# Performance work log

Measured on AMD Instinct MI355X. Metric: run time of the kernel, lower is better.

## Reference

```python
import jax, jax.numpy as jnp
import numpy as np

B, S, H = 2, 1024, 1024
E, I, K = 16, 512, 4
SHARED_I = 512 * 2  # moe_intermediate_size * moe_num_shared_experts
NORM_MIN = 1e-12


def _mlp(x, gw, uw, dw):
    # gated SiLU MLP: down(silu(gate(x)) * up(x))
    return (jax.nn.silu(x @ gw) * (x @ uw)) @ dw


def setup_inputs() -> dict:
    key = jax.random.key(0)
    ks = jax.random.split(key, 9)
    s = 0.02
    return {
        "hidden_states": jax.random.normal(ks[0], (B, S, H), jnp.float32),
        "gate_weight": jax.random.normal(ks[1], (H, E), jnp.float32) * s,
        "corr_bias": jnp.zeros((E,), jnp.float32),
        "gate_w": jax.random.normal(ks[2], (E, H, I), jnp.float32) * s,
        "up_w": jax.random.normal(ks[3], (E, H, I), jnp.float32) * s,
        "down_w": jax.random.normal(ks[4], (E, I, H), jnp.float32) * s,
        "shared_gate_w": jax.random.normal(ks[5], (H, SHARED_I), jnp.float32) * s,
        "shared_up_w": jax.random.normal(ks[6], (H, SHARED_I), jnp.float32) * s,
        "shared_down_w": jax.random.normal(ks[7], (SHARED_I, H), jnp.float32) * s,
    }


def reference(hidden_states, gate_weight, corr_bias, gate_w, up_w, down_w,
              shared_gate_w, shared_up_w, shared_down_w):
    b, s, h = hidden_states.shape
    x = hidden_states.reshape(-1, h)                      # [T, H]
    T = x.shape[0]

    # shared experts (full-capacity, always applied)
    shared_out = _mlp(x, shared_gate_w, shared_up_w, shared_down_w)

    # router in float32
    router_logits = x.astype(jnp.float32) @ gate_weight   # [T, E]
    probs = jax.nn.softmax(router_logits, axis=-1)
    # top-k on bias-corrected scores, weights gathered from uncorrected probs
    _, selected = jax.lax.top_k(probs + corr_bias[None, :], K)  # [T, K]
    rw = jnp.take_along_axis(probs, selected, axis=-1)          # [T, K]
    rw = rw / jnp.maximum(rw.sum(-1, keepdims=True), NORM_MIN)
    rw = rw.astype(x.dtype)

    # dense combine weights [T, E] (zero for unselected experts)
    cw = jnp.zeros((T, gate_weight.shape[1]), x.dtype)
    cw = cw.at[jnp.arange(T)[:, None], selected].add(rw)

    # grouped expert MLPs (full capacity, no token dropping)
    g = jnp.einsum('th,ehi->tei', x, gate_w)
    u = jnp.einsum('th,ehi->tei', x, up_w)
    eo = jnp.einsum('tei,eih->teh', jax.nn.silu(g) * u, down_w)
    final = jnp.einsum('teh,te->th', eo, cw) + shared_out

    return final.reshape(b, s, h), router_logits
```

## Files before the change

kernel.cpp:

```cpp
#include <hip/hip_runtime.h>
#include <hip/hip_bf16.h>

#define T_TOK 2048
#define H_DIM 1024
#define E_NUM 16
#define I_DIM 512
#define K_TOP 4
#define SI_DIM 1024

typedef __bf16 bf16x8 __attribute__((ext_vector_type(8)));
typedef __bf16 bf16x4 __attribute__((ext_vector_type(4)));
typedef float f32x4 __attribute__((ext_vector_type(4)));

#define GL2L(g, l)                                                                       \
  __builtin_amdgcn_global_load_lds((const __attribute__((address_space(1))) void*)(g),   \
                                   (__attribute__((address_space(3))) void*)(l), 16, 0, 0)
#define BAR() __builtin_amdgcn_s_barrier()

__global__ __launch_bounds__(256) void transpose_all_kernel(
    const float* __restrict__ gate_w, const float* __restrict__ up_w,
    const float* __restrict__ down_w, const float* __restrict__ sgw,
    const float* __restrict__ suw, const float* __restrict__ sdw,
    const float* __restrict__ gate_weight, __bf16* __restrict__ gw_t,
    __bf16* __restrict__ uw_t, __bf16* __restrict__ dw_t, __bf16* __restrict__ sgw_t,
    __bf16* __restrict__ suw_t, __bf16* __restrict__ sdw_t, float* __restrict__ gwt_f) {
  int tid = threadIdx.x;
  if (blockIdx.x >= 1728) {
    int b = blockIdx.x - 1728;
#pragma unroll
    for (int k = 0; k < 4; k++) {
      int idx = k * 4096 + b * 256 + tid;
      gwt_f[idx] = gate_weight[(idx & 1023) * E_NUM + (idx >> 10)];
    }
    return;
  }
  __shared__ float tile[64][65];
  for (int t = blockIdx.x; t < 6912; t += 1728) {
    const float* in;
    __bf16* out;
    int R, C, r0, c0;
    if (t < 4096) {
      bool g = t < 2048;
      int b = t & 2047;
      int z = b >> 7;
      int ti = b & 127;
      R = H_DIM;
      C = I_DIM;
      r0 = (ti >> 3) * 64;
      c0 = (ti & 7) * 64;
      size_t off = (size_t)z * R * C;
      in = (g ? gate_w : up_w) + off;
      out = (g ? gw_t : uw_t) + off;
    } else if (t < 6144) {
      int b = t - 4096;
      int z = b >> 7;
      int ti = b & 127;
      R = I_DIM;
      C = H_DIM;
      r0 = (ti >> 4) * 64;
      c0 = (ti & 15) * 64;
      size_t off = (size_t)z * R * C;
      in = down_w + off;
      out = dw_t + off;
    } else {
      int b = t - 6144;
      int m = b >> 8;
      int ti = b & 255;
      R = 1024;
      C = 1024;
      r0 = (ti >> 4) * 64;
      c0 = (ti & 15) * 64;
      in = m == 0 ? sgw : m == 1 ? suw : sdw;
      out = m == 0 ? sgw_t : m == 1 ? suw_t : sdw_t;
    }
#pragma unroll
    for (int q = 0; q < 4; q++) {
      int lin = q * 256 + tid;
      int row = lin >> 4, c4 = (lin & 15) * 4;
      float4 v = *(const float4*)(in + (size_t)(r0 + row) * C + c0 + c4);
      tile[row][c4] = v.x;
      tile[row][c4 + 1] = v.y;
      tile[row][c4 + 2] = v.z;
      tile[row][c4 + 3] = v.w;
    }
    __syncthreads();
    int c = tid >> 2, rb = (tid & 3) * 16;
    bf16x8 lo, hi;
#pragma unroll
    for (int i = 0; i < 8; i++) lo[i] = (__bf16)tile[rb + i][c];
#pragma unroll
    for (int i = 0; i < 8; i++) hi[i] = (__bf16)tile[rb + 8 + i][c];
    __bf16* op = out + (size_t)(c0 + c) * R + r0 + rb;
    *(bf16x8*)op = lo;
    *(bf16x8*)(op + 8) = hi;
    __syncthreads();
  }
}

__global__ __launch_bounds__(256) void router_kernel(
    const float* __restrict__ x, const float* __restrict__ gwt, const float* __restrict__ cbias,
    float* __restrict__ logits_out, __bf16* __restrict__ x_bf, int* __restrict__ selE,
    float* __restrict__ selW) {
  int t = blockIdx.x;
  int tid = threadIdx.x;
  int wid = tid >> 6, lane = tid & 63;
  int e = lane >> 2, cl = lane & 3;
  int c = wid * 4 + cl;
  const float* xr = x + (size_t)t * H_DIM + c * 64;
  const float* gr = gwt + (size_t)e * H_DIM + c * 64;
  float a0 = 0.f, a1 = 0.f, a2 = 0.f, a3 = 0.f;
#pragma unroll
  for (int j = 0; j < 16; j++) {
    float4 xv = *(const float4*)(xr + j * 4);
    float4 gv = *(const float4*)(gr + j * 4);
    if (e == 0) {
      bf16x4 o = {(__bf16)xv.x, (__bf16)xv.y, (__bf16)xv.z, (__bf16)xv.w};
      *(bf16x4*)(x_bf + (size_t)t * H_DIM + c * 64 + j * 4) = o;
    }
    a0 = fmaf(xv.x, gv.x, a0);
    a1 = fmaf(xv.y, gv.y, a1);
    a2 = fmaf(xv.z, gv.z, a2);
    a3 = fmaf(xv.w, gv.w, a3);
  }
  float a = (a0 + a1) + (a2 + a3);
  a += __shfl_xor(a, 1);
  a += __shfl_xor(a, 2);
  __shared__ float part[4][16];
  if (cl == 0) part[wid][e] = a;
  __syncthreads();
  if (wid != 0) return;
  float logit = -1e30f;
  if (lane < E_NUM)
    logit = (part[0][lane] + part[1][lane]) + (part[2][lane] + part[3][lane]);
  if (lane < E_NUM) logits_out[(size_t)t * E_NUM + lane] = logit;
  float m = logit;
#pragma unroll
  for (int mk = 8; mk >= 1; mk >>= 1) m = fmaxf(m, __shfl_xor(m, mk));
  float p = __expf(logit - m);
  float s = p;
#pragma unroll
  for (int mk = 8; mk >= 1; mk >>= 1) s += __shfl_xor(s, mk);
  p /= s;
  float score = (lane < E_NUM) ? p + cbias[lane] : -1e30f;
  int sel[K_TOP];
  float w[K_TOP];
#pragma unroll
  for (int k = 0; k < K_TOP; k++) {
    float bv = score;
    int bi = (lane < E_NUM) ? lane : 999;
#pragma unroll
    for (int mk = 1; mk <= 8; mk <<= 1) {
      float ov = __shfl_xor(bv, mk);
      int oi = __shfl_xor(bi, mk);
      if (ov > bv || (ov == bv && oi < bi)) {
        bv = ov;
        bi = oi;
      }
    }
    sel[k] = bi;
    w[k] = __shfl(p, bi);
    if (lane == bi) score = -1e30f;
  }
  if (lane == 0) {
    float wsum = fmaxf(w[0] + w[1] + w[2] + w[3], 1e-12f);
#pragma unroll
    for (int k = 0; k < K_TOP; k++) {
      selE[t * K_TOP + k] = sel[k];
      selW[t * K_TOP + k] = w[k] / wsum;
    }
  }
}

__global__ __launch_bounds__(1024) void count_place_kernel(
    const int* __restrict__ selE, int* __restrict__ counts, int* __restrict__ offs,
    int* __restrict__ slot_of_tk, int* __restrict__ tok_of_slot) {
  int tid = threadIdx.x;
  int wv = tid >> 6, lane = tid & 63;
  unsigned long long lt = (1ULL << lane) - 1ULL;
  __shared__ int wcnt[16][16];
  __shared__ int wbase[16][16];
  __shared__ int glob[16];
  __shared__ int offsh[16];
  if (tid < 16) glob[tid] = 0;
  __syncthreads();
  int ex[8], rk[8];
#pragma unroll
  for (int r = 0; r < 8; r++) {
    int e = selE[r * 1024 + tid];
    ex[r] = e;
    int rank = 0;
#pragma unroll
    for (int q = 0; q < 16; q++) {
      unsigned long long b = __ballot(e == q);
      int c = __popcll(b & lt);
      if (e == q) rank = c;
      if (lane == q) wcnt[wv][q] = __popcll(b);
    }
    __syncthreads();
    if (wv == 0 && lane < 16) {
      int run = glob[lane];
#pragma unroll
      for (int w = 0; w < 16; w++) {
        wbase[w][lane] = run;
        run += wcnt[w][lane];
      }
      glob[lane] = run;
    }
    __syncthreads();
    rk[r] = rank + wbase[wv][e];
    __syncthreads();
  }
  if (wv == 0 && lane == 0) {
    int s = 0;
#pragma unroll
    for (int q = 0; q < 16; q++) {
      offsh[q] = s;
      s += glob[q];
    }
  }
  __syncthreads();
  if (tid < 16) {
    counts[tid] = glob[tid];
    offs[tid] = offsh[tid];
  }
#pragma unroll
  for (int r = 0; r < 8; r++) {
    int entry = r * 1024 + tid;
    int slot = offsh[ex[r]] + rk[r];
    slot_of_tk[entry] = slot;
    tok_of_slot[slot] = entry >> 2;
  }
}

__global__ __launch_bounds__(256, 3) void gemm_stage1(
    const __bf16* __restrict__ x_bf, const int* __restrict__ tok_of_slot,
    const int* __restrict__ counts, const int* __restrict__ offs, const __bf16* __restrict__ gw_t,
    const __bf16* __restrict__ uw_t, const __bf16* __restrict__ sgw_t,
    const __bf16* __restrict__ suw_t, __bf16* __restrict__ he, __bf16* __restrict__ hs) {
  __shared__ __align__(16) __bf16 Alds[128 * 64];
  __shared__ __align__(16) __bf16 Bgl[2 * 64 * 64];
  __shared__ __align__(16) __bf16 Bul[2 * 64 * 64];
  int z = blockIdx.z, bx = blockIdx.x, m0 = blockIdx.y * 128;
  const __bf16 *Bg, *Bu;
  __bf16* Cp;
  const int* tokIdx;
  int rowOff, M, ldC, n0;
  if (z < E_NUM) {
    M = counts[z];
    if (m0 >= M) return;
    tokIdx = tok_of_slot;
    rowOff = offs[z];
    Bg = gw_t + (size_t)z * I_DIM * H_DIM;
    Bu = uw_t + (size_t)z * I_DIM * H_DIM;
    Cp = he;
    ldC = I_DIM;
    n0 = bx * 64;
  } else {
    tokIdx = nullptr;
    rowOff = 0;
    M = T_TOK;
    Bg = sgw_t;
    Bu = suw_t;
    Cp = hs;
    ldC = SI_DIM;
    n0 = (z - E_NUM) * 512 + bx * 64;
  }
  int tid = threadIdx.x;
  int wave = tid >> 6, lane = tid & 63;
  int rsub = lane >> 3, chunk = lane & 7;
  int sch = (chunk ^ rsub) * 8;
  size_t aB[4], bB[2];
#pragma unroll
  for (int j = 0; j < 4; j++) {
    int r = wave * 32 + j * 8 + rsub;
    int ar = m0 + r;
    ar = ar < M - 1 ? ar : M - 1;
    int grow = tokIdx ? tokIdx[rowOff + ar] : rowOff + ar;
    aB[j] = (size_t)grow * H_DIM + sch;
  }
#pragma unroll
  for (int j = 0; j < 2; j++) {
    int r = wave * 16 + j * 8 + rsub;
    bB[j] = (size_t)(n0 + r) * H_DIM + sch;
  }
  int wm = (wave >> 1) * 64, wn = (wave & 1) * 32;
  int rl = lane & 15, gq = lane >> 4;
  int xa = rl & 7;

  auto STAGE_A = [&](int k0) {
#pragma unroll
    for (int j = 0; j < 4; j++) GL2L(x_bf + aB[j] + k0, Alds + (wave * 32 + j * 8) * 64);
  };
  auto STAGE_B = [&](int k0, int buf) {
#pragma unroll
    for (int j = 0; j < 2; j++) {
      int ld = buf * 4096 + (wave * 16 + j * 8) * 64;
      GL2L(Bg + bB[j] + k0, Bgl + ld);
      GL2L(Bu + bB[j] + k0, Bul + ld);
    }
  };

  f32x4 accg[4][2] = {}, accu[4][2] = {};
  const int NT = H_DIM / 64;
  STAGE_A(0);
  STAGE_B(0, 0);
  int buf = 0;
  for (int t = 0; t < NT; ++t) {
    if (t + 1 < NT) {
      STAGE_B((t + 1) << 6, buf ^ 1);
      asm volatile("s_waitcnt vmcnt(4)" ::: "memory");
    } else {
      asm volatile("s_waitcnt vmcnt(0)" ::: "memory");
    }
    BAR();
    const __bf16* Bgr = Bgl + buf * 4096;
    const __bf16* Bur = Bul + buf * 4096;
#pragma unroll
    for (int s = 0; s < 2; s++) {
      int lc = ((s * 4 + gq) ^ xa) * 8;
      bf16x8 af[4], bg[2], bu[2];
#pragma unroll
      for (int m = 0; m < 4; m++) af[m] = *(const bf16x8*)&Alds[(wm + m * 16 + rl) * 64 + lc];
#pragma unroll
      for (int n = 0; n < 2; n++) {
        bg[n] = *(const bf16x8*)&Bgr[(wn + n * 16 + rl) * 64 + lc];
        bu[n] = *(const bf16x8*)&Bur[(wn + n * 16 + rl) * 64 + lc];
      }
#pragma unroll
      for (int m = 0; m < 4; m++)
#pragma unroll
        for (int n = 0; n < 2; n++) {
          accg[m][n] =
              __builtin_amdgcn_mfma_f32_16x16x32_bf16(af[m], bg[n], accg[m][n], 0, 0, 0);
          accu[m][n] =
              __builtin_amdgcn_mfma_f32_16x16x32_bf16(af[m], bu[n], accu[m][n], 0, 0, 0);
        }
    }
    BAR();
    if (t + 1 < NT) STAGE_A((t + 1) << 6);
    buf ^= 1;
  }
#pragma unroll
  for (int m = 0; m < 4; m++) {
#pragma unroll
    for (int b = 0; b < 4; b++) {
      int row = m0 + wm + m * 16 + gq * 4 + b;
      if (row < M) {
        size_t rb = (size_t)(rowOff + row) * ldC + n0 + wn + rl;
#pragma unroll
        for (int n = 0; n < 2; n++) {
          float g = accg[m][n][b];
          float u = accu[m][n][b];
          float h = g / (1.f + __expf(-g)) * u;
          Cp[rb + n * 16] = (__bf16)h;
        }
      }
    }
  }
}

__global__ __launch_bounds__(256, 4) void gemm_stage2(
    const __bf16* __restrict__ he, const __bf16* __restrict__ hs, const int* __restrict__ counts,
    const int* __restrict__ offs, const __bf16* __restrict__ dw_t,
    const __bf16* __restrict__ sdw_t, __bf16* __restrict__ eo, __bf16* __restrict__ so) {
  __shared__ __align__(16) __bf16 Alds[64 * 64];
  __shared__ __align__(16) __bf16 Blds[2 * 64 * 64];
  int z = blockIdx.z, bx = blockIdx.x, m0 = blockIdx.y * 64;
  const __bf16 *A, *Bp;
  __bf16* Cp;
  int rowOff, M, K;
  if (z < E_NUM) {
    M = counts[z];
    if (m0 >= M) return;
    A = he;
    rowOff = offs[z];
    K = I_DIM;
    Bp = dw_t + (size_t)z * H_DIM * I_DIM;
    Cp = eo;
  } else {
    A = hs;
    rowOff = 0;
    M = T_TOK;
    K = SI_DIM;
    Bp = sdw_t;
    Cp = so;
  }
  int n0 = bx * 64;
  int tid = threadIdx.x;
  int wave = tid >> 6, lane = tid & 63;
  int rsub = lane >> 3, chunk = lane & 7;
  int sch = (chunk ^ rsub) * 8;
  size_t aB[2], bB[2];
#pragma unroll
  for (int j = 0; j < 2; j++) {
    int r = wave * 16 + j * 8 + rsub;
    int ar = m0 + r;
    ar = ar < M - 1 ? ar : M - 1;
    aB[j] = (size_t)(rowOff + ar) * K + sch;
    bB[j] = (size_t)(n0 + r) * K + sch;
  }
  int wm = (wave >> 1) * 32, wn = (wave & 1) * 32;
  int rl = lane & 15, gq = lane >> 4;
  int xa = rl & 7;

  auto STAGE_A = [&](int k0) {
#pragma unroll
    for (int j = 0; j < 2; j++) GL2L(A + aB[j] + k0, Alds + (wave * 16 + j * 8) * 64);
  };
  auto STAGE_B = [&](int k0, int b) {
#pragma unroll
    for (int j = 0; j < 2; j++)
      GL2L(Bp + bB[j] + k0, Blds + b * 4096 + (wave * 16 + j * 8) * 64);
  };

  f32x4 acc[2][2] = {};
  const int NT = K >> 6;
  STAGE_A(0);
  STAGE_B(0, 0);
  int buf = 0;
  for (int t = 0; t < NT; ++t) {
    if (t + 1 < NT) {
      STAGE_B((t + 1) << 6, buf ^ 1);
      asm volatile("s_waitcnt vmcnt(2)" ::: "memory");
    } else {
      asm volatile("s_waitcnt vmcnt(0)" ::: "memory");
    }
    BAR();
    const __bf16* Br = Blds + buf * 4096;
#pragma unroll
    for (int s = 0; s < 2; s++) {
      int lc = ((s * 4 + gq) ^ xa) * 8;
      bf16x8 af[2], bfr[2];
#pragma unroll
      for (int m = 0; m < 2; m++) af[m] = *(const bf16x8*)&Alds[(wm + m * 16 + rl) * 64 + lc];
#pragma unroll
      for (int n = 0; n < 2; n++) bfr[n] = *(const bf16x8*)&Br[(wn + n * 16 + rl) * 64 + lc];
#pragma unroll
      for (int m = 0; m < 2; m++)
#pragma unroll
        for (int n = 0; n < 2; n++)
          acc[m][n] =
              __builtin_amdgcn_mfma_f32_16x16x32_bf16(af[m], bfr[n], acc[m][n], 0, 0, 0);
    }
    BAR();
    if (t + 1 < NT) STAGE_A((t + 1) << 6);
    buf ^= 1;
  }
#pragma unroll
  for (int m = 0; m < 2; m++) {
#pragma unroll
    for (int b = 0; b < 4; b++) {
      int row = m0 + wm + m * 16 + gq * 4 + b;
      if (row < M) {
        size_t rb = (size_t)(rowOff + row) * H_DIM + n0 + wn + rl;
#pragma unroll
        for (int n = 0; n < 2; n++) Cp[rb + n * 16] = (__bf16)acc[m][n][b];
      }
    }
  }
}

__global__ void combine_kernel(const __bf16* __restrict__ eo, const __bf16* __restrict__ so,
                               const int* __restrict__ slot_of_tk, const float* __restrict__ selW,
                               float* __restrict__ out) {
  int idx = blockIdx.x * blockDim.x + threadIdx.x;
  int t = idx >> 8;
  int h4 = (idx & 255) * 4;
  if (t >= T_TOK) return;
  bf16x4 sv = *(const bf16x4*)(so + (size_t)t * H_DIM + h4);
  float a0 = (float)sv[0], a1 = (float)sv[1], a2 = (float)sv[2], a3 = (float)sv[3];
#pragma unroll
  for (int k = 0; k < K_TOP; k++) {
    int slot = slot_of_tk[t * K_TOP + k];
    float w = selW[t * K_TOP + k];
    bf16x4 ev = *(const bf16x4*)(eo + (size_t)slot * H_DIM + h4);
    a0 += w * (float)ev[0];
    a1 += w * (float)ev[1];
    a2 += w * (float)ev[2];
    a3 += w * (float)ev[3];
  }
  *(float4*)(out + (size_t)t * H_DIM + h4) = make_float4(a0, a1, a2, a3);
}

extern "C" void kernel_launch(void* const* d_in, const int* in_sizes, int n_in, void* d_out,
                              int out_size, void* d_ws, size_t ws_size, hipStream_t stream) {
  const float* x = (const float*)d_in[0];
  const float* gate_weight = (const float*)d_in[1];
  const float* corr_bias = (const float*)d_in[2];
  const float* gate_w = (const float*)d_in[3];
  const float* up_w = (const float*)d_in[4];
  const float* down_w = (const float*)d_in[5];
  const float* sgw = (const float*)d_in[6];
  const float* suw = (const float*)d_in[7];
  const float* sdw = (const float*)d_in[8];
  float* out = (float*)d_out;
  float* logits_out = out + (size_t)T_TOK * H_DIM;

  char* wsb = (char*)d_ws;
  size_t o = 0;
  auto nxt = [&](size_t bytes) -> void* {
    void* p = wsb + o;
    o += (bytes + 1023) & ~(size_t)1023;
    return p;
  };
  const size_t EXP_ELE = (size_t)T_TOK * K_TOP * I_DIM;
  const size_t SH_ELE = (size_t)T_TOK * SI_DIM;
  __bf16* x_bf = (__bf16*)nxt((size_t)T_TOK * H_DIM * 2);
  __bf16* gw_t = (__bf16*)nxt((size_t)E_NUM * I_DIM * H_DIM * 2);
  __bf16* uw_t = (__bf16*)nxt((size_t)E_NUM * I_DIM * H_DIM * 2);
  __bf16* dw_t = (__bf16*)nxt((size_t)E_NUM * H_DIM * I_DIM * 2);
  __bf16* sgw_t = (__bf16*)nxt((size_t)SI_DIM * H_DIM * 2);
  __bf16* suw_t = (__bf16*)nxt((size_t)SI_DIM * H_DIM * 2);
  __bf16* sdw_t = (__bf16*)nxt((size_t)H_DIM * SI_DIM * 2);
  __bf16* h_all = (__bf16*)nxt((EXP_ELE + SH_ELE) * 2);
  __bf16* eo = (__bf16*)nxt((size_t)T_TOK * K_TOP * H_DIM * 2);
  __bf16* so = (__bf16*)nxt((size_t)T_TOK * H_DIM * 2);
  float* gwt_f = (float*)nxt((size_t)E_NUM * H_DIM * 4);
  int* counts = (int*)nxt(64);
  int* offs = (int*)nxt(128);
  int* selE = (int*)nxt((size_t)T_TOK * K_TOP * 4);
  float* selW = (float*)nxt((size_t)T_TOK * K_TOP * 4);
  int* slot_of_tk = (int*)nxt((size_t)T_TOK * K_TOP * 4);
  int* tok_of_slot = (int*)nxt((size_t)T_TOK * K_TOP * 4);
  __bf16* he = h_all;
  __bf16* hs = h_all + EXP_ELE;
  (void)ws_size;
  (void)in_sizes;
  (void)n_in;
  (void)out_size;

  transpose_all_kernel<<<1744, 256, 0, stream>>>(gate_w, up_w, down_w, sgw, suw, sdw,
                                                 gate_weight, gw_t, uw_t, dw_t, sgw_t, suw_t,
                                                 sdw_t, gwt_f);
  router_kernel<<<T_TOK, 256, 0, stream>>>(x, gwt_f, corr_bias, logits_out, x_bf, selE, selW);
  count_place_kernel<<<1, 1024, 0, stream>>>(selE, counts, offs, slot_of_tk, tok_of_slot);

  gemm_stage1<<<dim3(8, 16, E_NUM + 2), 256, 0, stream>>>(x_bf, tok_of_slot, counts, offs, gw_t,
                                                          uw_t, sgw_t, suw_t, he, hs);
  gemm_stage2<<<dim3(16, 32, E_NUM + 1), 256, 0, stream>>>(he, hs, counts, offs, dw_t, sdw_t, eo,
                                                           so);

  combine_kernel<<<(T_TOK * H_DIM / 4) / 256, 256, 0, stream>>>(eo, so, slot_of_tk, selW, out);
}
```

Baseline: 154.7 us.

## Rewrite weight transpose with bf16 swizzled LDS tile and one tile per block

The transpose kernel now converts to bf16 before staging in LDS, stores tiles in a XOR-swizzled layout, and reads pairs of columns as 32-bit words that are split with byte-perm instructions into two output rows. The grid-stride loop is replaced by launching one block per 64x64 tile. This halves LDS footprint and traffic, avoids bank conflicts without padding, and widens global loads and stores, at the cost of many more blocks to schedule.

```diff
diff --git a/kernel.cpp b/kernel.cpp
--- a/kernel.cpp
+++ b/kernel.cpp
@@ -25,8 +25,8 @@
     __bf16* __restrict__ uw_t, __bf16* __restrict__ dw_t, __bf16* __restrict__ sgw_t,
     __bf16* __restrict__ suw_t, __bf16* __restrict__ sdw_t, float* __restrict__ gwt_f) {
   int tid = threadIdx.x;
-  if (blockIdx.x >= 1728) {
-    int b = blockIdx.x - 1728;
+  if (blockIdx.x >= 6912) {
+    int b = blockIdx.x - 6912;
 #pragma unroll
     for (int k = 0; k < 4; k++) {
       int idx = k * 4096 + b * 256 + tid;
@@ -34,67 +34,79 @@
     }
     return;
   }
-  __shared__ float tile[64][65];
-  for (int t = blockIdx.x; t < 6912; t += 1728) {
-    const float* in;
-    __bf16* out;
-    int R, C, r0, c0;
-    if (t < 4096) {
-      bool g = t < 2048;
-      int b = t & 2047;
-      int z = b >> 7;
-      int ti = b & 127;
-      R = H_DIM;
-      C = I_DIM;
-      r0 = (ti >> 3) * 64;
-      c0 = (ti & 7) * 64;
-      size_t off = (size_t)z * R * C;
-      in = (g ? gate_w : up_w) + off;
-      out = (g ? gw_t : uw_t) + off;
-    } else if (t < 6144) {
-      int b = t - 4096;
-      int z = b >> 7;
-      int ti = b & 127;
-      R = I_DIM;
-      C = H_DIM;
-      r0 = (ti >> 4) * 64;
-      c0 = (ti & 15) * 64;
-      size_t off = (size_t)z * R * C;
-      in = down_w + off;
-      out = dw_t + off;
-    } else {
-      int b = t - 6144;
-      int m = b >> 8;
-      int ti = b & 255;
-      R = 1024;
-      C = 1024;
-      r0 = (ti >> 4) * 64;
-      c0 = (ti & 15) * 64;
-      in = m == 0 ? sgw : m == 1 ? suw : sdw;
-      out = m == 0 ? sgw_t : m == 1 ? suw_t : sdw_t;
-    }
-#pragma unroll
-    for (int q = 0; q < 4; q++) {
-      int lin = q * 256 + tid;
-      int row = lin >> 4, c4 = (lin & 15) * 4;
-      float4 v = *(const float4*)(in + (size_t)(r0 + row) * C + c0 + c4);
-      tile[row][c4] = v.x;
-      tile[row][c4 + 1] = v.y;
-      tile[row][c4 + 2] = v.z;
-      tile[row][c4 + 3] = v.w;
-    }
-    __syncthreads();
-    int c = tid >> 2, rb = (tid & 3) * 16;
-    bf16x8 lo, hi;
-#pragma unroll
-    for (int i = 0; i < 8; i++) lo[i] = (__bf16)tile[rb + i][c];
-#pragma unroll
-    for (int i = 0; i < 8; i++) hi[i] = (__bf16)tile[rb + 8 + i][c];
-    __bf16* op = out + (size_t)(c0 + c) * R + r0 + rb;
-    *(bf16x8*)op = lo;
-    *(bf16x8*)(op + 8) = hi;
-    __syncthreads();
-  }
+  __shared__ __align__(16) __bf16 tile[64 * 64];
+  int t = blockIdx.x;
+  const float* in;
+  __bf16* out;
+  int R, C, r0, c0;
+  if (t < 4096) {
+    bool g = t < 2048;
+    int b = t & 2047;
+    int z = b >> 7;
+    int ti = b & 127;
+    R = H_DIM;
+    C = I_DIM;
+    r0 = (ti >> 3) * 64;
+    c0 = (ti & 7) * 64;
+    size_t off = (size_t)z * R * C;
+    in = (g ? gate_w : up_w) + off;
+    out = (g ? gw_t : uw_t) + off;
+  } else if (t < 6144) {
+    int b = t - 4096;
+    int z = b >> 7;
+    int ti = b & 127;
+    R = I_DIM;
+    C = H_DIM;
+    r0 = (ti >> 4) * 64;
+    c0 = (ti & 15) * 64;
+    size_t off = (size_t)z * R * C;
+    in = down_w + off;
+    out = dw_t + off;
+  } else {
+    int b = t - 6144;
+    int m = b >> 8;
+    int ti = b & 255;
+    R = 1024;
+    C = 1024;
+    r0 = (ti >> 4) * 64;
+    c0 = (ti & 15) * 64;
+    in = m == 0 ? sgw : m == 1 ? suw : sdw;
+    out = m == 0 ? sgw_t : m == 1 ? suw_t : sdw_t;
+  }
+#pragma unroll
+  for (int q = 0; q < 2; q++) {
+    int lin8 = q * 256 + tid;
+    int row = lin8 >> 3, cb = lin8 & 7;
+    const float* ip = in + (size_t)(r0 + row) * C + c0 + cb * 8;
+    float4 v0 = *(const float4*)ip;
+    float4 v1 = *(const float4*)(ip + 4);
+    bf16x8 o;
+    o[0] = (__bf16)v0.x; o[1] = (__bf16)v0.y; o[2] = (__bf16)v0.z; o[3] = (__bf16)v0.w;
+    o[4] = (__bf16)v1.x; o[5] = (__bf16)v1.y; o[6] = (__bf16)v1.z; o[7] = (__bf16)v1.w;
+    int pcb = cb ^ ((row >> 3) & 7);
+    *(bf16x8*)&tile[row * 64 + pcb * 8] = o;
+  }
+  __syncthreads();
+  int p = tid >> 3, seg = tid & 7;
+  int c = p * 2;
+  const unsigned int* ldsw = (const unsigned int*)tile;
+  unsigned int d[8];
+#pragma unroll
+  for (int i = 0; i < 8; i++) {
+    int r = seg * 8 + i;
+    int pcb = (p >> 2) ^ seg;
+    d[i] = ldsw[r * 32 + pcb * 4 + (p & 3)];
+  }
+  unsigned int lo[4], hi[4];
+#pragma unroll
+  for (int j = 0; j < 4; j++) {
+    lo[j] = __builtin_amdgcn_perm(d[2 * j + 1], d[2 * j], 0x05040100u);
+    hi[j] = __builtin_amdgcn_perm(d[2 * j + 1], d[2 * j], 0x07060302u);
+  }
+  __bf16* op0 = out + (size_t)(c0 + c) * R + r0 + seg * 8;
+  __bf16* op1 = op0 + R;
+  *(uint4*)op0 = make_uint4(lo[0], lo[1], lo[2], lo[3]);
+  *(uint4*)op1 = make_uint4(hi[0], hi[1], hi[2], hi[3]);
 }
 
 __global__ __launch_bounds__(256) void router_kernel(
@@ -529,7 +541,7 @@
   (void)n_in;
   (void)out_size;
 
-  transpose_all_kernel<<<1744, 256, 0, stream>>>(gate_w, up_w, down_w, sgw, suw, sdw,
+  transpose_all_kernel<<<6928, 256, 0, stream>>>(gate_w, up_w, down_w, sgw, suw, sdw,
                                                  gate_weight, gw_t, uw_t, dw_t, sgw_t, suw_t,
                                                  sdw_t, gwt_f);
   router_kernel<<<T_TOK, 256, 0, stream>>>(x, gwt_f, corr_bias, logits_out, x_bf, selE, selW);
```

Result: no change. 154.6 us (-0.1%).
